# Kernel tuning notes

Hardware: AMD Instinct MI355X
Metric: run time of the kernel (lower is better)

The kernel has to match this reference:

```python
import jax, jax.numpy as jnp
import numpy as np


def setup_inputs() -> dict:
    key = jax.random.key(0)
    ks = jax.random.split(key, 8)
    b, m, e, d = 8, 4096, 2048, 128
    features = jax.random.normal(ks[0], (b, m, d), dtype=jnp.float32)
    # sparse-ish binary incidence matrix (nodes x hyperedges)
    inc_mat = (jax.random.uniform(ks[1], (b, m, e)) < 0.02).astype(jnp.float32)
    s = 1.0 / np.sqrt(d)
    return {
        "features": features,
        "inc_mat": inc_mat,
        "vc_Wa": jax.random.uniform(ks[2], (d, d), minval=-s, maxval=s),
        "vc_Wp": jax.random.uniform(ks[3], (d, d), minval=-s, maxval=s),
        "vc_alpha": jnp.float32(0.5),
        "ec_Wa": jax.random.uniform(ks[4], (d, d), minval=-s, maxval=s),
        "ec_Wp": jax.random.uniform(ks[5], (d, d), minval=-s, maxval=s),
        "ec_alpha": jnp.float32(0.5),
        "n_layers": 3,
    }


def _vertex_conv(feat, inc, Wa, Wp, alpha, prev=None):
    # feat: [b,m,d], inc: [b,m,e]
    att = feat @ Wa.T                                   # [b,m,d]
    e_att = jnp.einsum('bme,bmd->bed', inc, att)        # inc^T @ att
    attw = jax.nn.softmax(e_att, axis=1)                # softmax over edges
    agg = jnp.einsum('bme,bmd->bed', inc, feat)         # collapsed bmed outer-product + contract
    ef = (agg * attw) @ Wp.T                            # [b,e,d]
    if prev is not None:
        ef = alpha * prev + (1.0 - alpha) * ef
    return ef


def _edge_conv(inc, edge_feats, Wa, Wp, alpha, prev=None):
    # NOTE: original EdgeConv computes softmax attention_weights but never uses them (dead code).
    w = jnp.einsum('bed,bme->bmd', edge_feats, inc)     # inc @ edge_feats
    nf = w @ Wp.T                                       # [b,m,d]
    if prev is not None:
        nf = alpha * prev + (1.0 - alpha) * nf
    return nf


def reference(features, inc_mat, vc_Wa, vc_Wp, vc_alpha, ec_Wa, ec_Wp, ec_alpha, n_layers):
    edge_feats = _vertex_conv(features, inc_mat, vc_Wa, vc_Wp, vc_alpha)
    node_feats = _edge_conv(inc_mat, edge_feats, ec_Wa, ec_Wp, ec_alpha)
    for _ in range(1, n_layers):
        edge_feats = _vertex_conv(features, inc_mat, vc_Wa, vc_Wp, vc_alpha, prev=edge_feats)
        node_feats = _edge_conv(inc_mat, edge_feats, ec_Wa, ec_Wp, ec_alpha, prev=node_feats)
    return node_feats, edge_feats
```

## Files before the change

### kernel.cpp

```cpp
#include <hip/hip_runtime.h>

#define BB 8
#define MM 4096
#define EE 2048
#define DD 128

typedef _Float16 f16x8 __attribute__((ext_vector_type(8)));
typedef float    f32x4 __attribute__((ext_vector_type(4)));

__global__ __launch_bounds__(256) void transpose_to16(const float* __restrict__ src,
                                                      _Float16* __restrict__ dst,
                                                      int R, int C)
{
    __shared__ alignas(16) float tile[64 * 67];
    const int tilesC = C >> 6;
    const int r0 = (blockIdx.x / tilesC) << 6;
    const int c0 = (blockIdx.x % tilesC) << 6;
    const float* s = src + (size_t)blockIdx.y * R * C;
    _Float16*   d = dst + (size_t)blockIdx.y * R * C;
    const int t = threadIdx.x;
    #pragma unroll
    for (int i = 0; i < 4; i++){
        int idx = t + 256 * i;
        int r = idx >> 4, c4 = idx & 15;
        float4 v = *(const float4*)(s + (size_t)(r0 + r) * C + c0 + c4 * 4);
        tile[(c4 * 4 + 0) * 67 + r] = v.x;
        tile[(c4 * 4 + 1) * 67 + r] = v.y;
        tile[(c4 * 4 + 2) * 67 + r] = v.z;
        tile[(c4 * 4 + 3) * 67 + r] = v.w;
    }
    __syncthreads();
    #pragma unroll
    for (int i = 0; i < 2; i++){
        int idx = t + 256 * i;
        int row = idx >> 3, rb = idx & 7;
        f16x8 h;
        #pragma unroll
        for (int j = 0; j < 8; j++) h[j] = (_Float16)tile[row * 67 + rb * 8 + j];
        *(f16x8*)(d + (size_t)(c0 + row) * R + r0 + rb * 8) = h;
    }
}

__global__ __launch_bounds__(256, 1) void fused_gemm1(const float* __restrict__ inc,
                                                      const _Float16* __restrict__ featT,
                                                      unsigned long long* __restrict__ bitsX,
                                                      float* __restrict__ p)
{
    __shared__ alignas(16) char smem[36864];

    const int x = blockIdx.x;
    const int b = blockIdx.y;
    const int z = blockIdx.z;
    const int t = threadIdx.x, lane = t & 63, w = t >> 6;
    const int fr = lane & 15, q = lane >> 4, q8 = q * 8;

    const int e0 = x * 256;
    const int ew0 = e0 + w * 64;
    const _Float16* dp = featT + (size_t)b * 128 * MM;
    const float* ip = inc + (size_t)b * MM * EE + ew0 + lane;
    unsigned long long* bxp = bitsX + ((size_t)b * 32 + (x * 4 + w)) * MM;

    f32x4 acc[4][8] = {};
    uint4 rd[4];
    float val[64];

    auto loadg = [&](int k0){
        #pragma unroll
        for (int i = 0; i < 4; i++){
            int idx = t + 256 * i;
            int dd = idx >> 3, kb = idx & 7;
            rd[i] = *(const uint4*)(dp + (size_t)dd * MM + k0 + kb * 8);
        }
        const float* rp = ip + (size_t)k0 * EE;
        #pragma unroll
        for (int j = 0; j < 64; j++) val[j] = rp[(size_t)j * EE];
    };
    auto stage = [&](int buf, int k0){
        _Float16* lD = (_Float16*)(smem + buf * 16384);
        unsigned long long* lBits = (unsigned long long*)(smem + 32768 + buf * 2048);
        #pragma unroll
        for (int i = 0; i < 4; i++){
            int idx = t + 256 * i;
            int dd = idx >> 3, kb = idx & 7;
            *(uint4*)&lD[dd * 64 + ((kb ^ (dd & 7)) * 8)] = rd[i];
        }
        unsigned long long wbits = 0;
        #pragma unroll
        for (int j = 0; j < 64; j++){
            unsigned long long bal = __ballot(val[j] != 0.0f);
            wbits = (lane == j) ? bal : wbits;
        }
        bxp[k0 + lane] = wbits;
        unsigned long long wT = 0;
        #pragma unroll
        for (int ei = 0; ei < 64; ei++){
            unsigned long long bal = __ballot((wbits >> ei) & 1ull);
            wT = (lane == ei) ? bal : wT;
        }
        lBits[w * 64 + lane] = wT;
    };
    auto compute = [&](int buf){
        const _Float16* lD = (const _Float16*)(smem + buf * 16384);
        const uint2* lBits = (const uint2*)(smem + 32768 + buf * 2048);
        uint2 bw[4];
        f16x8 af[4][2];
        #pragma unroll
        for (int s = 0; s < 4; s++) bw[s] = lBits[w * 64 + s * 16 + fr];
        #pragma unroll
        for (int s = 0; s < 4; s++)
            #pragma unroll
            for (int h = 0; h < 2; h++){
                unsigned word = h ? bw[s].y : bw[s].x;
                unsigned byte = (word >> q8) & 0xFFu;
                #pragma unroll
                for (int j = 0; j < 8; j++)
                    af[s][h][j] = ((byte >> j) & 1u) ? (_Float16)1.0f : (_Float16)0.0f;
            }
        #pragma unroll
        for (int h = 0; h < 2; h++)
            #pragma unroll
            for (int c = 0; c < 8; c++){
                int drow = c * 16 + fr;
                f16x8 bf = *(const f16x8*)&lD[drow * 64 + (((h * 4 + q) ^ (drow & 7)) * 8)];
                #pragma unroll
                for (int s = 0; s < 4; s++)
                    acc[s][c] = __builtin_amdgcn_mfma_f32_16x16x32_f16(af[s][h], bf, acc[s][c], 0, 0, 0);
            }
    };

    const int kbase = z * 1024;
    loadg(kbase); stage(0, kbase); __syncthreads();
    for (int c = 0; c < 16; c++){
        if (c + 1 < 16) loadg(kbase + (c + 1) * 64);
        compute(c & 1);
        if (c + 1 < 16) stage((c + 1) & 1, kbase + (c + 1) * 64);
        __syncthreads();
    }

    float* sT = (float*)smem;
    float* op = p + (size_t)z * 2097152 + ((size_t)b * EE + e0) * 128;
    for (int ph = 0; ph < 4; ph++){
        __syncthreads();
        if (w == ph){
            #pragma unroll
            for (int s = 0; s < 4; s++)
                #pragma unroll
                for (int c = 0; c < 8; c++)
                    #pragma unroll
                    for (int reg = 0; reg < 4; reg++)
                        sT[(s * 16 + q * 4 + reg) * 132 + c * 16 + fr] = acc[s][c][reg];
        }
        __syncthreads();
        #pragma unroll
        for (int i = 0; i < 8; i++){
            int idx = t + 256 * i;
            int lrow = idx >> 5, c4 = idx & 31;
            float4 v = *(const float4*)&sT[lrow * 132 + c4 * 4];
            *(float4*)(op + (size_t)(ph * 64 + lrow) * 128 + c4 * 4) = v;
        }
    }
}

__global__ __launch_bounds__(256) void bitgemm2_fused(const unsigned long long* __restrict__ bitsX,
                                                      const _Float16* __restrict__ PT,
                                                      const _Float16* __restrict__ Wc16,
                                                      float* __restrict__ node)
{
    __shared__ alignas(16) char smem[66560];
    const int b = blockIdx.y;
    const int m0 = blockIdx.x * 64;
    const unsigned long long* bxp = bitsX + (size_t)b * 32 * MM;
    const _Float16* dp = PT + (size_t)b * 128 * EE;
    float* op = node + ((size_t)b * MM + m0) * 128;

    const int t = threadIdx.x, lane = t & 63, w = t >> 6;
    const int fr = lane & 15, q = lane >> 4, q8 = q * 8;

    _Float16* lWc = (_Float16*)(smem + 33792);
    #pragma unroll
    for (int i = 0; i < 8; i++){
        int idx = t + 256 * i;
        int n = idx >> 4, kb = idx & 15;
        *(uint4*)&lWc[n * 128 + ((kb ^ (n & 7)) * 8)] =
            *(const uint4*)(Wc16 + (size_t)n * 128 + kb * 8);
    }

    f32x4 acc[8] = {};
    uint4 rd[4];
    unsigned long long rb;

    auto loadg = [&](int kg){
        #pragma unroll
        for (int i = 0; i < 4; i++){
            int idx = t + 256 * i;
            int dd = idx >> 3, kb = idx & 7;
            rd[i] = *(const uint4*)(dp + (size_t)dd * EE + kg + kb * 8);
        }
        if (t < 64) rb = bxp[(size_t)(kg >> 6) * MM + m0 + t];
    };
    auto stage = [&](int buf){
        _Float16* lD = (_Float16*)(smem + buf * 16384);
        unsigned long long* lB = (unsigned long long*)(smem + 32768 + buf * 512);
        #pragma unroll
        for (int i = 0; i < 4; i++){
            int idx = t + 256 * i;
            int dd = idx >> 3, kb = idx & 7;
            *(uint4*)&lD[dd * 64 + ((kb ^ (dd & 7)) * 8)] = rd[i];
        }
        if (t < 64) lB[t] = rb;
    };
    auto compute = [&](int buf){
        const _Float16* lD = (const _Float16*)(smem + buf * 16384);
        const uint2* lB = (const uint2*)(smem + 32768 + buf * 512);
        uint2 bw = lB[w * 16 + fr];
        #pragma unroll
        for (int h = 0; h < 2; h++){
            unsigned word = h ? bw.y : bw.x;
            unsigned byte = (word >> q8) & 0xFFu;
            f16x8 af;
            #pragma unroll
            for (int j = 0; j < 8; j++)
                af[j] = ((byte >> j) & 1u) ? (_Float16)1.0f : (_Float16)0.0f;
            #pragma unroll
            for (int c = 0; c < 8; c++){
                int drow = c * 16 + fr;
                f16x8 bf = *(const f16x8*)&lD[drow * 64 + (((h * 4 + q) ^ (drow & 7)) * 8)];
                acc[c] = __builtin_amdgcn_mfma_f32_16x16x32_f16(af, bf, acc[c], 0, 0, 0);
            }
        }
    };

    loadg(0); stage(0); __syncthreads();
    for (int c = 0; c < 32; c++){
        if (c + 1 < 32) loadg((c + 1) * 64);
        compute(c & 1);
        if (c + 1 < 32) stage((c + 1) & 1);
        __syncthreads();
    }

    _Float16* sQ = (_Float16*)smem;
    #pragma unroll
    for (int c = 0; c < 8; c++){
        #pragma unroll
        for (int reg = 0; reg < 4; reg++){
            int row = w * 16 + q * 4 + reg;
            int col = c * 16 + fr;
            sQ[row * 128 + (((col >> 3) ^ (row & 7)) * 8) + (col & 7)] = (_Float16)acc[c][reg];
        }
    }
    f32x4 acc2[8] = {};
    #pragma unroll
    for (int kk = 0; kk < 4; kk++){
        int arow = w * 16 + fr;
        f16x8 a2 = *(const f16x8*)&sQ[arow * 128 + (((kk * 4 + q) ^ (arow & 7)) * 8)];
        #pragma unroll
        for (int c = 0; c < 8; c++){
            int n = c * 16 + fr;
            f16x8 b2 = *(const f16x8*)&lWc[n * 128 + (((kk * 4 + q) ^ (n & 7)) * 8)];
            acc2[c] = __builtin_amdgcn_mfma_f32_16x16x32_f16(a2, b2, acc2[c], 0, 0, 0);
        }
    }
    __syncthreads();
    float* sD = (float*)smem;
    #pragma unroll
    for (int c = 0; c < 8; c++)
        #pragma unroll
        for (int reg = 0; reg < 4; reg++)
            sD[(w * 16 + q * 4 + reg) * 132 + c * 16 + fr] = acc2[c][reg];
    __syncthreads();
    #pragma unroll
    for (int i = 0; i < 8; i++){
        int idx = t + 256 * i;
        int lrow = idx >> 5, c4 = idx & 31;
        float4 v = *(const float4*)&sD[lrow * 132 + c4 * 4];
        *(float4*)(op + (size_t)lrow * 128 + c4 * 4) = v;
    }
}

__global__ __launch_bounds__(256) void rowmm_sum4(const float* __restrict__ p,
                                                  const float* __restrict__ W,
                                                  float* aggOut,
                                                  float* __restrict__ C)
{
    __shared__ alignas(16) float lA[32][132];
    __shared__ alignas(16) float lW[64][140];
    const int t = threadIdx.x;
    const int row0 = blockIdx.x * 32;
    const float4* P4 = (const float4*)p;
    const float4* W4 = (const float4*)W;
    float4* A4 = (float4*)aggOut;
    const size_t SS = 2097152 / 4;

    #pragma unroll
    for (int i = 0; i < 4; i++){
        int idx = t + 256 * i;
        int r = idx >> 5, k4 = idx & 31;
        size_t gi = (size_t)(row0 + r) * 32 + k4;
        float4 a = P4[gi], b = P4[gi + SS], c = P4[gi + 2 * SS], d = P4[gi + 3 * SS];
        float4 s = make_float4(a.x + b.x + c.x + d.x, a.y + b.y + c.y + d.y,
                               a.z + b.z + c.z + d.z, a.w + b.w + c.w + d.w);
        *(float4*)&lA[r][k4 * 4] = s;
        A4[gi] = s;
    }
    const int qq = t >> 5, cc = t & 31;

    #pragma unroll
    for (int ph = 0; ph < 2; ph++){
        __syncthreads();
        #pragma unroll
        for (int i = 0; i < 8; i++){
            int idx = t + 256 * i;
            int c = idx >> 5, k4 = idx & 31;
            *(float4*)&lW[c][k4 * 4] = W4[(size_t)(ph * 64 + c) * 32 + k4];
        }
        __syncthreads();
        float s[4][2] = {};
        for (int k4 = 0; k4 < 32; k4++){
            float4 w0 = *(const float4*)&lW[cc][k4 * 4];
            float4 w1 = *(const float4*)&lW[cc + 32][k4 * 4];
            #pragma unroll
            for (int j = 0; j < 4; j++){
                float4 a = *(const float4*)&lA[qq + 8 * j][k4 * 4];
                s[j][0] += a.x * w0.x + a.y * w0.y + a.z * w0.z + a.w * w0.w;
                s[j][1] += a.x * w1.x + a.y * w1.y + a.z * w1.z + a.w * w1.w;
            }
        }
        #pragma unroll
        for (int j = 0; j < 4; j++){
            size_t ro = (size_t)(row0 + qq + 8 * j) * DD + ph * 64;
            C[ro + cc]      = s[j][0];
            C[ro + cc + 32] = s[j][1];
        }
    }
}

__global__ __launch_bounds__(256) void rowmm(const float* A,
                                             const float* __restrict__ W,
                                             float* C)
{
    __shared__ alignas(16) float lA[32][132];
    __shared__ alignas(16) float lW[64][140];
    const int t = threadIdx.x;
    const int row0 = blockIdx.x * 32;
    const float4* A4 = (const float4*)A;
    const float4* W4 = (const float4*)W;

    #pragma unroll
    for (int i = 0; i < 4; i++){
        int idx = t + 256 * i;
        int r = idx >> 5, k4 = idx & 31;
        *(float4*)&lA[r][k4 * 4] = A4[(size_t)(row0 + r) * 32 + k4];
    }
    const int qq = t >> 5, cc = t & 31;

    #pragma unroll
    for (int ph = 0; ph < 2; ph++){
        __syncthreads();
        #pragma unroll
        for (int i = 0; i < 8; i++){
            int idx = t + 256 * i;
            int c = idx >> 5, k4 = idx & 31;
            *(float4*)&lW[c][k4 * 4] = W4[(size_t)(ph * 64 + c) * 32 + k4];
        }
        __syncthreads();
        float s[4][2] = {};
        for (int k4 = 0; k4 < 32; k4++){
            float4 w0 = *(const float4*)&lW[cc][k4 * 4];
            float4 w1 = *(const float4*)&lW[cc + 32][k4 * 4];
            #pragma unroll
            for (int j = 0; j < 4; j++){
                float4 a = *(const float4*)&lA[qq + 8 * j][k4 * 4];
                s[j][0] += a.x * w0.x + a.y * w0.y + a.z * w0.z + a.w * w0.w;
                s[j][1] += a.x * w1.x + a.y * w1.y + a.z * w1.z + a.w * w1.w;
            }
        }
        #pragma unroll
        for (int j = 0; j < 4; j++){
            size_t ro = (size_t)(row0 + qq + 8 * j) * DD + ph * 64;
            C[ro + cc]      = s[j][0];
            C[ro + cc + 32] = s[j][1];
        }
    }
}

__global__ __launch_bounds__(256) void wc_mm16(const float* __restrict__ eWp,
                                               const float* __restrict__ vWp,
                                               _Float16* __restrict__ Wc16)
{
    int i = blockIdx.x * 2 + (threadIdx.x >> 7);
    int j = threadIdx.x & 127;
    float acc = 0.f;
    for (int k = 0; k < 128; k++)
        acc += eWp[i * 128 + k] * vWp[k * 128 + j];
    Wc16[i * 128 + j] = (_Float16)acc;
}

__global__ __launch_bounds__(256) void sm_part(const float* __restrict__ eatt,
                                               float* __restrict__ part)
{
    const int b = blockIdx.x, slab = blockIdx.y;
    const int t = threadIdx.x;
    const int dl = t & 127, eh = t >> 7;
    const size_t base = (size_t)b * EE * DD + dl;
    const int e0 = slab * 256;
    float m = -1e30f;
    for (int s = 0; s < 128; s++)
        m = fmaxf(m, eatt[base + (size_t)(e0 + eh + 2 * s) * DD]);
    float l = 0.f;
    for (int s = 0; s < 128; s++)
        l += __expf(eatt[base + (size_t)(e0 + eh + 2 * s) * DD] - m);
    __shared__ float red[2][128][2];
    red[eh][dl][0] = m; red[eh][dl][1] = l;
    __syncthreads();
    if (t < 128){
        float m0 = red[0][t][0], l0 = red[0][t][1];
        float m1 = red[1][t][0], l1 = red[1][t][1];
        float M = fmaxf(m0, m1);
        float L = l0 * __expf(m0 - M) + l1 * __expf(m1 - M);
        float* pp = part + ((size_t)(b * 8 + slab) * DD + t) * 2;
        pp[0] = M; pp[1] = L;
    }
}

__global__ __launch_bounds__(256) void sm_apply(float* __restrict__ eatt,
                                                const float* __restrict__ agg,
                                                const float* __restrict__ part)
{
    const int b = blockIdx.x, sl = blockIdx.y;
    const int t = threadIdx.x;
    __shared__ float mv[128], iv[128];
    if (t < 128){
        float mbuf[8], lbuf[8];
        float M = -1e30f;
        #pragma unroll
        for (int s = 0; s < 8; s++){
            const float* pp = part + ((size_t)(b * 8 + s) * DD + t) * 2;
            mbuf[s] = pp[0]; lbuf[s] = pp[1];
            M = fmaxf(M, mbuf[s]);
        }
        float L = 0.f;
        #pragma unroll
        for (int s = 0; s < 8; s++) L += lbuf[s] * __expf(mbuf[s] - M);
        mv[t] = M; iv[t] = 1.f / L;
    }
    __syncthreads();
    const int dl = t & 127, eh = t >> 7;
    const size_t base = (size_t)b * EE * DD + dl;
    const int e0 = sl * 128;
    for (int s = 0; s < 64; s++){
        size_t ix = base + (size_t)(e0 + eh + 2 * s) * DD;
        eatt[ix] = agg[ix] * __expf(eatt[ix] - mv[dl]) * iv[dl];
    }
}

extern "C" void kernel_launch(void* const* d_in, const int* in_sizes, int n_in,
                              void* d_out, int out_size, void* d_ws, size_t ws_size,
                              hipStream_t stream)
{
    const float* feat = (const float*)d_in[0];
    const float* inc  = (const float*)d_in[1];
    const float* vWa  = (const float*)d_in[2];
    const float* vWp  = (const float*)d_in[3];
    const float* eWp  = (const float*)d_in[6];

    float* node_out = (float*)d_out;
    float* edge_out = node_out + (size_t)BB * MM * DD;

    char* w = (char*)d_ws;
    unsigned long long* bitsX = (unsigned long long*)w;
    float* pk  = (float*)(w + ((size_t)8 << 20));
    float* agg = pk;
    _Float16* PT = (_Float16*)(w + ((size_t)16 << 20));
    _Float16* Wc16 = (_Float16*)(w + ((size_t)40 << 20));

    _Float16* featT = (_Float16*)node_out;
    float* eattP = node_out + 2097152;
    float* part  = edge_out;

    dim3 blk(256);

    transpose_to16<<<dim3((MM / 64) * (DD / 64), BB), blk, 0, stream>>>(feat, featT, MM, DD);
    wc_mm16<<<dim3(64), blk, 0, stream>>>(eWp, vWp, Wc16);
    fused_gemm1<<<dim3(EE / 256, BB, 4), blk, 0, stream>>>(inc, featT, bitsX, pk);
    rowmm_sum4<<<dim3(BB * EE / 32), blk, 0, stream>>>(pk, vWa, agg, eattP);
    sm_part <<<dim3(BB, 8),  blk, 0, stream>>>(eattP, part);
    sm_apply<<<dim3(BB, 16), blk, 0, stream>>>(eattP, agg, part);
    rowmm<<<dim3(BB * EE / 32), blk, 0, stream>>>(eattP, vWp, edge_out);
    transpose_to16<<<dim3((EE / 64) * (DD / 64), BB), blk, 0, stream>>>(eattP, PT, EE, DD);
    bitgemm2_fused<<<dim3(MM / 64, BB), blk, 0, stream>>>(bitsX, PT, Wc16, node_out);
}
```

Baseline: 565.2 us.

## Enlarge tiles in bitgemm2, rowmm kernels and split softmax partials finer

bitgemm2_fused now handles 128 rows per block, two MFMA row-tiles per wave sharing each B fragment, which halves the grid and reuses the staged PT tiles across twice as many rows. rowmm and rowmm_sum4 move to 64-row tiles with a 4x4 register micro-tile per thread, an XOR-swizzled shared layout and float4 stores. sm_part uses 16 slabs that preload their values into registers instead of reading global memory twice. The cost is higher register pressure and fewer blocks, which can reduce occupancy and load balance.

```diff
diff --git a/kernel.cpp b/kernel.cpp
--- a/kernel.cpp
+++ b/kernel.cpp
@@ -166,9 +166,9 @@
                                                       const _Float16* __restrict__ Wc16,
                                                       float* __restrict__ node)
 {
-    __shared__ alignas(16) char smem[66560];
+    __shared__ alignas(16) char smem[67584];
     const int b = blockIdx.y;
-    const int m0 = blockIdx.x * 64;
+    const int m0 = blockIdx.x * 128;
     const unsigned long long* bxp = bitsX + (size_t)b * 32 * MM;
     const _Float16* dp = PT + (size_t)b * 128 * EE;
     float* op = node + ((size_t)b * MM + m0) * 128;
@@ -176,7 +176,7 @@
     const int t = threadIdx.x, lane = t & 63, w = t >> 6;
     const int fr = lane & 15, q = lane >> 4, q8 = q * 8;
 
-    _Float16* lWc = (_Float16*)(smem + 33792);
+    _Float16* lWc = (_Float16*)(smem + 34816);
     #pragma unroll
     for (int i = 0; i < 8; i++){
         int idx = t + 256 * i;
@@ -185,7 +185,7 @@
             *(const uint4*)(Wc16 + (size_t)n * 128 + kb * 8);
     }
 
-    f32x4 acc[8] = {};
+    f32x4 acc[2][8] = {};
     uint4 rd[4];
     unsigned long long rb;
 
@@ -196,36 +196,42 @@
             int dd = idx >> 3, kb = idx & 7;
             rd[i] = *(const uint4*)(dp + (size_t)dd * EE + kg + kb * 8);
         }
-        if (t < 64) rb = bxp[(size_t)(kg >> 6) * MM + m0 + t];
+        if (t < 128) rb = bxp[(size_t)(kg >> 6) * MM + m0 + t];
     };
     auto stage = [&](int buf){
         _Float16* lD = (_Float16*)(smem + buf * 16384);
-        unsigned long long* lB = (unsigned long long*)(smem + 32768 + buf * 512);
+        unsigned long long* lB = (unsigned long long*)(smem + 32768 + buf * 1024);
         #pragma unroll
         for (int i = 0; i < 4; i++){
             int idx = t + 256 * i;
             int dd = idx >> 3, kb = idx & 7;
             *(uint4*)&lD[dd * 64 + ((kb ^ (dd & 7)) * 8)] = rd[i];
         }
-        if (t < 64) lB[t] = rb;
+        if (t < 128) lB[t] = rb;
     };
     auto compute = [&](int buf){
         const _Float16* lD = (const _Float16*)(smem + buf * 16384);
-        const uint2* lB = (const uint2*)(smem + 32768 + buf * 512);
-        uint2 bw = lB[w * 16 + fr];
+        const uint2* lB = (const uint2*)(smem + 32768 + buf * 1024);
+        uint2 bw0 = lB[w * 32 + fr];
+        uint2 bw1 = lB[w * 32 + 16 + fr];
         #pragma unroll
         for (int h = 0; h < 2; h++){
-            unsigned word = h ? bw.y : bw.x;
-            unsigned byte = (word >> q8) & 0xFFu;
-            f16x8 af;
-            #pragma unroll
-            for (int j = 0; j < 8; j++)
-                af[j] = ((byte >> j) & 1u) ? (_Float16)1.0f : (_Float16)0.0f;
+            unsigned word0 = h ? bw0.y : bw0.x;
+            unsigned word1 = h ? bw1.y : bw1.x;
+            unsigned byte0 = (word0 >> q8) & 0xFFu;
+            unsigned byte1 = (word1 >> q8) & 0xFFu;
+            f16x8 af0, af1;
+            #pragma unroll
+            for (int j = 0; j < 8; j++){
+                af0[j] = ((byte0 >> j) & 1u) ? (_Float16)1.0f : (_Float16)0.0f;
+                af1[j] = ((byte1 >> j) & 1u) ? (_Float16)1.0f : (_Float16)0.0f;
+            }
             #pragma unroll
             for (int c = 0; c < 8; c++){
                 int drow = c * 16 + fr;
                 f16x8 bf = *(const f16x8*)&lD[drow * 64 + (((h * 4 + q) ^ (drow & 7)) * 8)];
-                acc[c] = __builtin_amdgcn_mfma_f32_16x16x32_f16(af, bf, acc[c], 0, 0, 0);
+                acc[0][c] = __builtin_amdgcn_mfma_f32_16x16x32_f16(af0, bf, acc[0][c], 0, 0, 0);
+                acc[1][c] = __builtin_amdgcn_mfma_f32_16x16x32_f16(af1, bf, acc[1][c], 0, 0, 0);
             }
         }
     };
@@ -240,36 +246,42 @@
 
     _Float16* sQ = (_Float16*)smem;
     #pragma unroll
-    for (int c = 0; c < 8; c++){
-        #pragma unroll
-        for (int reg = 0; reg < 4; reg++){
-            int row = w * 16 + q * 4 + reg;
-            int col = c * 16 + fr;
-            sQ[row * 128 + (((col >> 3) ^ (row & 7)) * 8) + (col & 7)] = (_Float16)acc[c][reg];
-        }
-    }
-    f32x4 acc2[8] = {};
+    for (int u = 0; u < 2; u++)
+        #pragma unroll
+        for (int c = 0; c < 8; c++)
+            #pragma unroll
+            for (int reg = 0; reg < 4; reg++){
+                int row = w * 32 + u * 16 + q * 4 + reg;
+                int col = c * 16 + fr;
+                sQ[row * 128 + (((col >> 3) ^ (row & 7)) * 8) + (col & 7)] = (_Float16)acc[u][c][reg];
+            }
+    f32x4 acc2[2][8] = {};
     #pragma unroll
     for (int kk = 0; kk < 4; kk++){
-        int arow = w * 16 + fr;
-        f16x8 a2 = *(const f16x8*)&sQ[arow * 128 + (((kk * 4 + q) ^ (arow & 7)) * 8)];
+        int arow0 = w * 32 + fr;
+        int arow1 = w * 32 + 16 + fr;
+        f16x8 a20 = *(const f16x8*)&sQ[arow0 * 128 + (((kk * 4 + q) ^ (arow0 & 7)) * 8)];
+        f16x8 a21 = *(const f16x8*)&sQ[arow1 * 128 + (((kk * 4 + q) ^ (arow1 & 7)) * 8)];
         #pragma unroll
         for (int c = 0; c < 8; c++){
             int n = c * 16 + fr;
             f16x8 b2 = *(const f16x8*)&lWc[n * 128 + (((kk * 4 + q) ^ (n & 7)) * 8)];
-            acc2[c] = __builtin_amdgcn_mfma_f32_16x16x32_f16(a2, b2, acc2[c], 0, 0, 0);
+            acc2[0][c] = __builtin_amdgcn_mfma_f32_16x16x32_f16(a20, b2, acc2[0][c], 0, 0, 0);
+            acc2[1][c] = __builtin_amdgcn_mfma_f32_16x16x32_f16(a21, b2, acc2[1][c], 0, 0, 0);
         }
     }
     __syncthreads();
     float* sD = (float*)smem;
     #pragma unroll
-    for (int c = 0; c < 8; c++)
-        #pragma unroll
-        for (int reg = 0; reg < 4; reg++)
-            sD[(w * 16 + q * 4 + reg) * 132 + c * 16 + fr] = acc2[c][reg];
+    for (int u = 0; u < 2; u++)
+        #pragma unroll
+        for (int c = 0; c < 8; c++)
+            #pragma unroll
+            for (int reg = 0; reg < 4; reg++)
+                sD[(w * 32 + u * 16 + q * 4 + reg) * 132 + c * 16 + fr] = acc2[u][c][reg];
     __syncthreads();
     #pragma unroll
-    for (int i = 0; i < 8; i++){
+    for (int i = 0; i < 16; i++){
         int idx = t + 256 * i;
         int lrow = idx >> 5, c4 = idx & 31;
         float4 v = *(const float4*)&sD[lrow * 132 + c4 * 4];
@@ -282,27 +294,28 @@
                                                   float* aggOut,
                                                   float* __restrict__ C)
 {
-    __shared__ alignas(16) float lA[32][132];
-    __shared__ alignas(16) float lW[64][140];
+    __shared__ alignas(16) float lA[64][132];
+    __shared__ alignas(16) float lW[64][132];
     const int t = threadIdx.x;
-    const int row0 = blockIdx.x * 32;
+    const int row0 = blockIdx.x * 64;
     const float4* P4 = (const float4*)p;
     const float4* W4 = (const float4*)W;
     float4* A4 = (float4*)aggOut;
     const size_t SS = 2097152 / 4;
 
     #pragma unroll
-    for (int i = 0; i < 4; i++){
+    for (int i = 0; i < 8; i++){
         int idx = t + 256 * i;
         int r = idx >> 5, k4 = idx & 31;
         size_t gi = (size_t)(row0 + r) * 32 + k4;
         float4 a = P4[gi], b = P4[gi + SS], c = P4[gi + 2 * SS], d = P4[gi + 3 * SS];
         float4 s = make_float4(a.x + b.x + c.x + d.x, a.y + b.y + c.y + d.y,
                                a.z + b.z + c.z + d.z, a.w + b.w + c.w + d.w);
-        *(float4*)&lA[r][k4 * 4] = s;
+        *(float4*)&lA[r][((k4 ^ (r >> 3)) & 31) * 4] = s;
         A4[gi] = s;
     }
-    const int qq = t >> 5, cc = t & 31;
+    const int rr = t >> 4, cg = t & 15;
+    const int keyA = rr >> 1, keyW = cg >> 1;
 
     #pragma unroll
     for (int ph = 0; ph < 2; ph++){
@@ -310,27 +323,28 @@
         #pragma unroll
         for (int i = 0; i < 8; i++){
             int idx = t + 256 * i;
-            int c = idx >> 5, k4 = idx & 31;
-            *(float4*)&lW[c][k4 * 4] = W4[(size_t)(ph * 64 + c) * 32 + k4];
-        }
-        __syncthreads();
-        float s[4][2] = {};
+            int cN = idx >> 5, k4 = idx & 31;
+            *(float4*)&lW[cN][((k4 ^ (cN >> 3)) & 31) * 4] = W4[(size_t)(ph * 64 + cN) * 32 + k4];
+        }
+        __syncthreads();
+        float s[4][4] = {};
         for (int k4 = 0; k4 < 32; k4++){
-            float4 w0 = *(const float4*)&lW[cc][k4 * 4];
-            float4 w1 = *(const float4*)&lW[cc + 32][k4 * 4];
-            #pragma unroll
-            for (int j = 0; j < 4; j++){
-                float4 a = *(const float4*)&lA[qq + 8 * j][k4 * 4];
-                s[j][0] += a.x * w0.x + a.y * w0.y + a.z * w0.z + a.w * w0.w;
-                s[j][1] += a.x * w1.x + a.y * w1.y + a.z * w1.z + a.w * w1.w;
-            }
-        }
-        #pragma unroll
-        for (int j = 0; j < 4; j++){
-            size_t ro = (size_t)(row0 + qq + 8 * j) * DD + ph * 64;
-            C[ro + cc]      = s[j][0];
-            C[ro + cc + 32] = s[j][1];
-        }
+            float4 wv[4];
+            #pragma unroll
+            for (int jc = 0; jc < 4; jc++)
+                wv[jc] = *(const float4*)&lW[cg * 4 + jc][((k4 ^ keyW) & 31) * 4];
+            #pragma unroll
+            for (int i = 0; i < 4; i++){
+                float4 a = *(const float4*)&lA[rr * 4 + i][((k4 ^ keyA) & 31) * 4];
+                #pragma unroll
+                for (int jc = 0; jc < 4; jc++)
+                    s[i][jc] += a.x * wv[jc].x + a.y * wv[jc].y + a.z * wv[jc].z + a.w * wv[jc].w;
+            }
+        }
+        #pragma unroll
+        for (int i = 0; i < 4; i++)
+            *(float4*)&C[(size_t)(row0 + rr * 4 + i) * DD + ph * 64 + cg * 4] =
+                make_float4(s[i][0], s[i][1], s[i][2], s[i][3]);
     }
 }
 
@@ -338,20 +352,21 @@
                                              const float* __restrict__ W,
                                              float* C)
 {
-    __shared__ alignas(16) float lA[32][132];
-    __shared__ alignas(16) float lW[64][140];
+    __shared__ alignas(16) float lA[64][132];
+    __shared__ alignas(16) float lW[64][132];
     const int t = threadIdx.x;
-    const int row0 = blockIdx.x * 32;
+    const int row0 = blockIdx.x * 64;
     const float4* A4 = (const float4*)A;
     const float4* W4 = (const float4*)W;
 
     #pragma unroll
-    for (int i = 0; i < 4; i++){
+    for (int i = 0; i < 8; i++){
         int idx = t + 256 * i;
         int r = idx >> 5, k4 = idx & 31;
-        *(float4*)&lA[r][k4 * 4] = A4[(size_t)(row0 + r) * 32 + k4];
-    }
-    const int qq = t >> 5, cc = t & 31;
+        *(float4*)&lA[r][((k4 ^ (r >> 3)) & 31) * 4] = A4[(size_t)(row0 + r) * 32 + k4];
+    }
+    const int rr = t >> 4, cg = t & 15;
+    const int keyA = rr >> 1, keyW = cg >> 1;
 
     #pragma unroll
     for (int ph = 0; ph < 2; ph++){
@@ -359,27 +374,28 @@
         #pragma unroll
         for (int i = 0; i < 8; i++){
             int idx = t + 256 * i;
-            int c = idx >> 5, k4 = idx & 31;
-            *(float4*)&lW[c][k4 * 4] = W4[(size_t)(ph * 64 + c) * 32 + k4];
-        }
-        __syncthreads();
-        float s[4][2] = {};
+            int cN = idx >> 5, k4 = idx & 31;
+            *(float4*)&lW[cN][((k4 ^ (cN >> 3)) & 31) * 4] = W4[(size_t)(ph * 64 + cN) * 32 + k4];
+        }
+        __syncthreads();
+        float s[4][4] = {};
         for (int k4 = 0; k4 < 32; k4++){
-            float4 w0 = *(const float4*)&lW[cc][k4 * 4];
-            float4 w1 = *(const float4*)&lW[cc + 32][k4 * 4];
-            #pragma unroll
-            for (int j = 0; j < 4; j++){
-                float4 a = *(const float4*)&lA[qq + 8 * j][k4 * 4];
-                s[j][0] += a.x * w0.x + a.y * w0.y + a.z * w0.z + a.w * w0.w;
-                s[j][1] += a.x * w1.x + a.y * w1.y + a.z * w1.z + a.w * w1.w;
-            }
-        }
-        #pragma unroll
-        for (int j = 0; j < 4; j++){
-            size_t ro = (size_t)(row0 + qq + 8 * j) * DD + ph * 64;
-            C[ro + cc]      = s[j][0];
-            C[ro + cc + 32] = s[j][1];
-        }
+            float4 wv[4];
+            #pragma unroll
+            for (int jc = 0; jc < 4; jc++)
+                wv[jc] = *(const float4*)&lW[cg * 4 + jc][((k4 ^ keyW) & 31) * 4];
+            #pragma unroll
+            for (int i = 0; i < 4; i++){
+                float4 a = *(const float4*)&lA[rr * 4 + i][((k4 ^ keyA) & 31) * 4];
+                #pragma unroll
+                for (int jc = 0; jc < 4; jc++)
+                    s[i][jc] += a.x * wv[jc].x + a.y * wv[jc].y + a.z * wv[jc].z + a.w * wv[jc].w;
+            }
+        }
+        #pragma unroll
+        for (int i = 0; i < 4; i++)
+            *(float4*)&C[(size_t)(row0 + rr * 4 + i) * DD + ph * 64 + cg * 4] =
+                make_float4(s[i][0], s[i][1], s[i][2], s[i][3]);
     }
 }
 
@@ -402,13 +418,17 @@
     const int t = threadIdx.x;
     const int dl = t & 127, eh = t >> 7;
     const size_t base = (size_t)b * EE * DD + dl;
-    const int e0 = slab * 256;
+    const int e0 = slab * 128;
+    float v[64];
+    #pragma unroll
+    for (int s = 0; s < 64; s++)
+        v[s] = eatt[base + (size_t)(e0 + eh + 2 * s) * DD];
     float m = -1e30f;
-    for (int s = 0; s < 128; s++)
-        m = fmaxf(m, eatt[base + (size_t)(e0 + eh + 2 * s) * DD]);
+    #pragma unroll
+    for (int s = 0; s < 64; s++) m = fmaxf(m, v[s]);
     float l = 0.f;
-    for (int s = 0; s < 128; s++)
-        l += __expf(eatt[base + (size_t)(e0 + eh + 2 * s) * DD] - m);
+    #pragma unroll
+    for (int s = 0; s < 64; s++) l += __expf(v[s] - m);
     __shared__ float red[2][128][2];
     red[eh][dl][0] = m; red[eh][dl][1] = l;
     __syncthreads();
@@ -417,7 +437,7 @@
         float m1 = red[1][t][0], l1 = red[1][t][1];
         float M = fmaxf(m0, m1);
         float L = l0 * __expf(m0 - M) + l1 * __expf(m1 - M);
-        float* pp = part + ((size_t)(b * 8 + slab) * DD + t) * 2;
+        float* pp = part + ((size_t)(b * 16 + slab) * DD + t) * 2;
         pp[0] = M; pp[1] = L;
     }
 }
@@ -430,17 +450,17 @@
     const int t = threadIdx.x;
     __shared__ float mv[128], iv[128];
     if (t < 128){
-        float mbuf[8], lbuf[8];
+        float mbuf[16], lbuf[16];
         float M = -1e30f;
         #pragma unroll
-        for (int s = 0; s < 8; s++){
-            const float* pp = part + ((size_t)(b * 8 + s) * DD + t) * 2;
+        for (int s = 0; s < 16; s++){
+            const float* pp = part + ((size_t)(b * 16 + s) * DD + t) * 2;
             mbuf[s] = pp[0]; lbuf[s] = pp[1];
             M = fmaxf(M, mbuf[s]);
         }
         float L = 0.f;
         #pragma unroll
-        for (int s = 0; s < 8; s++) L += lbuf[s] * __expf(mbuf[s] - M);
+        for (int s = 0; s < 16; s++) L += lbuf[s] * __expf(mbuf[s] - M);
         mv[t] = M; iv[t] = 1.f / L;
     }
     __syncthreads();
@@ -482,10 +502,10 @@
     transpose_to16<<<dim3((MM / 64) * (DD / 64), BB), blk, 0, stream>>>(feat, featT, MM, DD);
     wc_mm16<<<dim3(64), blk, 0, stream>>>(eWp, vWp, Wc16);
     fused_gemm1<<<dim3(EE / 256, BB, 4), blk, 0, stream>>>(inc, featT, bitsX, pk);
-    rowmm_sum4<<<dim3(BB * EE / 32), blk, 0, stream>>>(pk, vWa, agg, eattP);
-    sm_part <<<dim3(BB, 8),  blk, 0, stream>>>(eattP, part);
+    rowmm_sum4<<<dim3(BB * EE / 64), blk, 0, stream>>>(pk, vWa, agg, eattP);
+    sm_part <<<dim3(BB, 16), blk, 0, stream>>>(eattP, part);
     sm_apply<<<dim3(BB, 16), blk, 0, stream>>>(eattP, agg, part);
-    rowmm<<<dim3(BB * EE / 32), blk, 0, stream>>>(eattP, vWp, edge_out);
+    rowmm<<<dim3(BB * EE / 64), blk, 0, stream>>>(eattP, vWp, edge_out);
     transpose_to16<<<dim3((EE / 64) * (DD / 64), BB), blk, 0, stream>>>(eattP, PT, EE, DD);
-    bitgemm2_fused<<<dim3(MM / 64, BB), blk, 0, stream>>>(bitsX, PT, Wc16, node_out);
-}
+    bitgemm2_fused<<<dim3(MM / 128, BB), blk, 0, stream>>>(bitsX, PT, Wc16, node_out);
+}
```

Result: faster. 529.1 us (-6.4%).
